# Kernel optimization log

Hardware: AMD Instinct MI355X
Metric: run time of the kernel (lower is better)

Reference implementation:

```python
import jax, jax.numpy as jnp
import numpy as np

LN_EPS = 1e-5


def _ln(x, g, b):
    mu = jnp.mean(x, -1, keepdims=True)
    xc = x - mu
    inv = jax.lax.rsqrt(jnp.mean(xc * xc, -1, keepdims=True) + LN_EPS)
    return xc * inv * g + b


def _subm_conv(x, nbr, W, b):
    # Submanifold 3D conv via rulebook gather-GEMM-accumulate.
    # x: [N, Cin], nbr: [N, K] neighbor row ids (-1 = missing), W: [K, Cin, Cout], b: [Cout]
    N = x.shape[0]
    xp = jnp.concatenate([x, jnp.zeros((1, x.shape[1]), x.dtype)], 0)  # sentinel zero row
    idx = jnp.where(nbr < 0, N, nbr)  # missing neighbors -> zero row
    acc0 = jnp.zeros((N, W.shape[-1]), x.dtype) + b
    def body(acc, xs):
        i, Wk = xs  # i: [N], Wk: [Cin, Cout]
        return acc + xp[i] @ Wk, None
    acc, _ = jax.lax.scan(body, acc0, (idx.T, W))
    return acc


def _blk1(x, W, b, g, be):  # 1x1x1 SubMConv + LN + ReLU
    return jax.nn.relu(_ln(x @ W + b, g, be))


def _blk3(x, nbr, W, b, g, be):  # 3x3x3 SubMConv + LN + ReLU
    return jax.nn.relu(_ln(_subm_conv(x, nbr, W, b), g, be))


def setup_inputs() -> dict:
    rng = np.random.default_rng(0)
    B, D, Npb, K = 2, 160, 131072, 27
    dim, half = 64, 32
    # Build random sparse voxel set and the rulebook (neighbor table) like spconv does.
    lookup = np.full((B, D, D, D), -1, np.int64)
    coords = np.zeros((B * Npb, 3), np.int64)
    for b in range(B):
        lin = np.sort(rng.choice(D * D * D, size=Npb, replace=False))
        z, y, x = np.unravel_index(lin, (D, D, D))
        rows = np.arange(b * Npb, (b + 1) * Npb)
        lookup[b, z, y, x] = rows
        coords[rows] = np.stack([z, y, x], 1)
    bidx = np.repeat(np.arange(B), Npb)
    offs = np.stack(np.meshgrid(np.arange(-1, 2), np.arange(-1, 2), np.arange(-1, 2), indexing="ij"), -1).reshape(K, 3)
    nz = coords[:, None, :] + offs[None]  # [N, K, 3]
    valid = ((nz >= 0) & (nz < D)).all(-1)
    nzc = np.clip(nz, 0, D - 1)
    nbr = lookup[bidx[:, None], nzc[..., 0], nzc[..., 1], nzc[..., 2]]
    nbr = np.where(valid, nbr, -1).astype(np.int32)

    key = jax.random.key(0)
    ks = iter(jax.random.split(key, 16))
    f32 = jnp.float32
    d = {"voxel_features": jax.random.normal(next(ks), (B * Npb, dim), f32),
         "nbr_idx": jnp.asarray(nbr)}
    def lnp(c):
        return jnp.ones((c,), f32), jnp.zeros((c,), f32)
    d["W1"] = 0.05 * jax.random.normal(next(ks), (dim, dim), f32); d["b1"] = jnp.zeros((dim,), f32); d["g1"], d["be1"] = lnp(dim)
    d["W2"] = 0.05 * jax.random.normal(next(ks), (dim, dim), f32); d["b2"] = jnp.zeros((dim,), f32); d["g2"], d["be2"] = lnp(dim)
    d["W3"] = 0.05 * jax.random.normal(next(ks), (K, dim, half), f32); d["b3"] = jnp.zeros((half,), f32); d["g3"], d["be3"] = lnp(half)
    d["W4"] = 0.05 * jax.random.normal(next(ks), (K, half, half), f32); d["b4"] = jnp.zeros((half,), f32); d["g4"], d["be4"] = lnp(half)
    d["W5"] = 0.05 * jax.random.normal(next(ks), (K, half, half), f32); d["b5"] = jnp.zeros((half,), f32); d["g5"], d["be5"] = lnp(half)
    d["W6"] = 0.05 * jax.random.normal(next(ks), (K, half, half), f32); d["b6"] = jnp.zeros((half,), f32); d["g6"], d["be6"] = lnp(half)
    d["W7"] = 0.05 * jax.random.normal(next(ks), (4 * dim, dim), f32); d["b7"] = jnp.zeros((dim,), f32); d["g7"], d["be7"] = lnp(dim)
    return d


def reference(voxel_features, nbr_idx,
              W1, b1, g1, be1, W2, b2, g2, be2,
              W3, b3, g3, be3, W4, b4, g4, be4,
              W5, b5, g5, be5, W6, b6, g6, be6,
              W7, b7, g7, be7):
    x = voxel_features
    f1 = _blk1(x, W1, b1, g1, be1)
    f2 = _blk1(x, W2, b2, g2, be2)
    feats = [f1, f2]
    f2 = _blk3(f2, nbr_idx, W3, b3, g3, be3); feats.append(f2)
    f2 = _blk3(f2, nbr_idx, W4, b4, g4, be4); feats.append(f2)
    f2 = _blk3(f2, nbr_idx, W5, b5, g5, be5); feats.append(f2)
    f2 = _blk3(f2, nbr_idx, W6, b6, g6, be6); feats.append(f2)
    cat = jnp.concatenate(feats, -1)  # [N, 4*dim]
    return _blk1(cat, W7, b7, g7, be7)
```

## Files before the change

### kernel.cpp

```cpp
#include <hip/hip_runtime.h>

typedef __attribute__((ext_vector_type(4))) float  float4_;
typedef __attribute__((ext_vector_type(8))) short  short8;
typedef __attribute__((ext_vector_type(8))) __bf16 bf16x8;
typedef __attribute__((ext_vector_type(4))) unsigned uint4_;

__device__ inline unsigned short f2bf(float f) {
    unsigned u = __builtin_bit_cast(unsigned, f);
    u += 0x7FFFu + ((u >> 16) & 1u);
    return (unsigned short)(u >> 16);
}

__device__ inline float4_ mfma16(bf16x8 a, bf16x8 b, float4_ c) {
    return __builtin_amdgcn_mfma_f32_16x16x32_bf16(a, b, c, 0, 0, 0);
}

__device__ inline void packW_one(const float* __restrict__ src, unsigned short* __restrict__ dst,
                                 int cin, int cout, int e) {
    int f = e >> 9, i = e & 511, lane = i >> 3, t = i & 7;
    int ntn = cout >> 4, ctn = cin >> 5;
    int nt = f % ntn;
    int rest = f / ntn;
    int ct = rest % ctn;
    int k = rest / ctn;
    int c = ct * 32 + (lane >> 4) * 8 + t;
    int j = nt * 16 + (lane & 15);
    dst[e] = f2bf(src[(k * cin + c) * cout + j]);
}

__global__ void pack_all_kernel(
    const float* __restrict__ W1, const float* __restrict__ W2,
    const float* __restrict__ W3, const float* __restrict__ W4,
    const float* __restrict__ W5, const float* __restrict__ W6,
    const float* __restrict__ W7,
    unsigned short* cat, unsigned short* Wp12, unsigned short* Wp3,
    unsigned short* Wp4, unsigned short* Wp5, unsigned short* Wp6,
    unsigned short* Wp7, int N) {
    int e = blockIdx.x * 256 + threadIdx.x;
    if (e < 8192) {
        int f = e >> 9, i = e & 511, lane = i >> 3, t = i & 7;
        int nt = f & 7, ct = f >> 3;
        int c = ct * 32 + (lane >> 4) * 8 + t;
        int j = nt * 16 + (lane & 15);
        float v = (j < 64) ? W1[c * 64 + j] : W2[c * 64 + (j - 64)];
        Wp12[e] = f2bf(v);
        return;
    }
    e -= 8192;
    if (e < 57344) { if (e < 55296) packW_one(W3, Wp3, 64, 32, e); else Wp3[e] = 0; return; }
    e -= 57344;
    if (e < 28672) { if (e < 27648) packW_one(W4, Wp4, 32, 32, e); else Wp4[e] = 0; return; }
    e -= 28672;
    if (e < 28672) { if (e < 27648) packW_one(W5, Wp5, 32, 32, e); else Wp5[e] = 0; return; }
    e -= 28672;
    if (e < 28672) { if (e < 27648) packW_one(W6, Wp6, 32, 32, e); else Wp6[e] = 0; return; }
    e -= 28672;
    if (e < 16384) { packW_one(W7, Wp7, 256, 64, e); return; }
    e -= 16384;
    if (e < 128) ((unsigned*)(cat + (size_t)N * 256))[e] = 0;
}

__global__ __launch_bounds__(256) void plan_kernel(const int* __restrict__ nbr,
                                                   unsigned int* __restrict__ kmask,
                                                   unsigned int* __restrict__ cidx,
                                                   unsigned char* __restrict__ ktab, int N) {
    __shared__ int snb[6912];
    __shared__ unsigned tm[16];
    int tid = threadIdx.x;
    if (tid < 16) tm[tid] = 0u;
    __syncthreads();
    long base = (long)blockIdx.x * 6912;
#pragma unroll
    for (int i = 0; i < 27; i++) {
        int j = i * 256 + tid;
        int v = nbr[base + j];
        snb[j] = v;
        if (v >= 0) {
            unsigned r = (unsigned)j / 27u;
            unsigned k = (unsigned)j - r * 27u;
            atomicOr(&tm[r >> 4], 1u << k);
        }
    }
    __syncthreads();
    int g = tid >> 4, r = tid & 15;
    unsigned m = tm[g];
    int t = blockIdx.x * 16 + g;
    unsigned* cp = cidx + (long)t * 448;
    int j = 0;
#pragma unroll
    for (int k = 0; k < 27; k++) {
        if (m >> k & 1u) {
            int v = snb[(g * 16 + r) * 27 + k];
            cp[j * 16 + r] = (unsigned)(v < 0 ? N : v) * 512u;
            j++;
        }
    }
    for (; j < 28; j++) cp[j * 16 + r] = (unsigned)N * 512u;
    if (r == 0) {
        kmask[t] = m;
        unsigned char* kt = ktab + (long)t * 32;
        int jj = 0;
#pragma unroll
        for (int k = 0; k < 27; k++)
            if (m >> k & 1u) kt[jj++] = (unsigned char)k;
        for (; jj < 32; jj++) kt[jj] = 27;
    }
}

__global__ __launch_bounds__(256) void blk12_kernel(
    const float* __restrict__ x, unsigned short* cat,
    const unsigned short* __restrict__ Wp,
    const float* __restrict__ b1, const float* __restrict__ g1, const float* __restrict__ be1,
    const float* __restrict__ b2, const float* __restrict__ g2, const float* __restrict__ be2) {
    int tid = threadIdx.x, lane = tid & 63, wv = tid >> 6;
    int l15 = lane & 15, q = lane >> 4;
    long base = ((long)blockIdx.x * 4 + wv) * 16;

    float4_ acc[8];
#pragma unroll
    for (int i = 0; i < 8; i++) acc[i] = (float4_){0.f, 0.f, 0.f, 0.f};

#pragma unroll
    for (int kt = 0; kt < 2; kt++) {
        const float* xp = x + (base + l15) * 64 + kt * 32 + q * 8;
        float4_ f0 = *(const float4_*)xp;
        float4_ f1 = *(const float4_*)(xp + 4);
        short8 as;
        as[0] = (short)f2bf(f0[0]); as[1] = (short)f2bf(f0[1]);
        as[2] = (short)f2bf(f0[2]); as[3] = (short)f2bf(f0[3]);
        as[4] = (short)f2bf(f1[0]); as[5] = (short)f2bf(f1[1]);
        as[6] = (short)f2bf(f1[2]); as[7] = (short)f2bf(f1[3]);
        bf16x8 a = __builtin_bit_cast(bf16x8, as);
        const unsigned short* wp = Wp + (size_t)kt * 8 * 512;
#pragma unroll
        for (int nt = 0; nt < 8; nt++) {
            bf16x8 w = *(const bf16x8*)(wp + nt * 512 + lane * 8);
            acc[nt] = mfma16(a, w, acc[nt]);
        }
    }

    float bc[8], gc[8], bec[8];
#pragma unroll
    for (int nt = 0; nt < 8; nt++) {
        int j = nt * 16 + l15;
        if (j < 64) { bc[nt] = b1[j]; gc[nt] = g1[j]; bec[nt] = be1[j]; }
        else        { bc[nt] = b2[j - 64]; gc[nt] = g2[j - 64]; bec[nt] = be2[j - 64]; }
    }

#pragma unroll
    for (int r = 0; r < 4; r++) {
        long row = base + q * 4 + r;
        float v[8], s0 = 0.f, s1 = 0.f, q0 = 0.f, q1 = 0.f;
#pragma unroll
        for (int nt = 0; nt < 4; nt++) { v[nt] = acc[nt][r] + bc[nt]; s0 += v[nt]; q0 += v[nt] * v[nt]; }
#pragma unroll
        for (int nt = 4; nt < 8; nt++) { v[nt] = acc[nt][r] + bc[nt]; s1 += v[nt]; q1 += v[nt] * v[nt]; }
#pragma unroll
        for (int m = 1; m < 16; m <<= 1) {
            s0 += __shfl_xor(s0, m); q0 += __shfl_xor(q0, m);
            s1 += __shfl_xor(s1, m); q1 += __shfl_xor(q1, m);
        }
        float mu0 = s0 * (1.f / 64), var0 = q0 * (1.f / 64) - mu0 * mu0, inv0 = rsqrtf(var0 + 1e-5f);
        float mu1 = s1 * (1.f / 64), var1 = q1 * (1.f / 64) - mu1 * mu1, inv1 = rsqrtf(var1 + 1e-5f);
        unsigned short* cp = cat + row * 256;
#pragma unroll
        for (int nt = 0; nt < 4; nt++) {
            float y = fmaxf((v[nt] - mu0) * inv0 * gc[nt] + bec[nt], 0.f);
            cp[nt * 16 + l15] = f2bf(y);
        }
#pragma unroll
        for (int nt = 4; nt < 8; nt++) {
            float y = fmaxf((v[nt] - mu1) * inv1 * gc[nt] + bec[nt], 0.f);
            cp[nt * 16 + l15] = f2bf(y);
        }
    }
}

template <int CT, int D, int NS>
__device__ __forceinline__ void conv_core(
    float4_ acc[2], const char* catb, const unsigned* cx,
    const unsigned* kt8, const unsigned short* wl) {
    bf16x8 f[D + 1][CT];
    bf16x8 wr[3][CT][2];
    unsigned cv[3];

#define KB(k) ((kt8[(k) >> 2] >> (((k) & 3) * 8)) & 0xFFu)

    unsigned cv0[D + 2];
#pragma unroll
    for (int j = 0; j < D + 2; j++) cv0[j] = cx[j * 16];

#pragma unroll
    for (int kk = 0; kk < 2; kk++) {
        unsigned wo = KB(kk) * (CT * 1024u);
#pragma unroll
        for (int ct = 0; ct < CT; ct++)
#pragma unroll
            for (int nt = 0; nt < 2; nt++)
                wr[kk][ct][nt] = *(const bf16x8*)(wl + wo + (ct * 2 + nt) * 512);
    }

#pragma unroll
    for (int j = 0; j < D; j++) {
#pragma unroll
        for (int ct = 0; ct < CT; ct++)
            f[j][ct] = *(const bf16x8*)(catb + (size_t)cv0[j] + ct * 64);
    }
    cv[D % 3] = cv0[D];
    cv[(D + 1) % 3] = cv0[D + 1];

#pragma unroll
    for (int k = 0; k < NS; k++) {
        if (k + 2 < NS) {
            unsigned wo = KB(k + 2) * (CT * 1024u);
#pragma unroll
            for (int ct = 0; ct < CT; ct++)
#pragma unroll
                for (int nt = 0; nt < 2; nt++)
                    wr[(k + 2) % 3][ct][nt] = *(const bf16x8*)(wl + wo + (ct * 2 + nt) * 512);
        }
        if (k + D < NS) {
            unsigned voff = cv[(k + D) % 3];
#pragma unroll
            for (int ct = 0; ct < CT; ct++)
                f[(k + D) % (D + 1)][ct] = *(const bf16x8*)(catb + (size_t)voff + ct * 64);
        }
        if (k + D + 2 < NS) cv[(k + D + 2) % 3] = cx[(k + D + 2) * 16];
#pragma unroll
        for (int ct = 0; ct < CT; ct++) {
            acc[0] = mfma16(f[k % (D + 1)][ct], wr[k % 3][ct][0], acc[0]);
            acc[1] = mfma16(f[k % (D + 1)][ct], wr[k % 3][ct][1], acc[1]);
        }
    }
#undef KB
}

template <int CT, int D>
__global__ __launch_bounds__(256) void conv_kernel(
    unsigned short* cat, const unsigned int* __restrict__ cidx,
    const unsigned char* __restrict__ ktab,
    const unsigned int* __restrict__ kmask,
    const unsigned short* __restrict__ Wp,
    const float* __restrict__ bb, const float* __restrict__ gg, const float* __restrict__ bee,
    int in_off, int out_off, int N) {
    int tid = threadIdx.x, lane = tid & 63, wv = tid >> 6;
    int l15 = lane & 15, q = lane >> 4;

    int cpx = (int)(gridDim.x >> 3);
    int sb = ((int)blockIdx.x & 7) * cpx + ((int)blockIdx.x >> 3);
    int t = sb * 4 + wv;
    long base = (long)t * 16;

    unsigned m = __builtin_amdgcn_readfirstlane(kmask[t]);
    int trips = (__popc(m) + 3) >> 2;

    const char* catb = (const char*)cat + (size_t)in_off * 2 + q * 16;
    const unsigned* cx = cidx + (long)t * 448 + l15;
    const unsigned short* wl = Wp + lane * 8;

    uint4_ kv0 = *(const uint4_*)(ktab + (long)t * 32);
    uint4_ kv1 = *(const uint4_*)(ktab + (long)t * 32 + 16);
    unsigned kt8[8] = {kv0[0], kv0[1], kv0[2], kv0[3], kv1[0], kv1[1], kv1[2], kv1[3]};

    float4_ acc[2];
    acc[0] = (float4_){0.f, 0.f, 0.f, 0.f};
    acc[1] = (float4_){0.f, 0.f, 0.f, 0.f};

    switch (trips) {
        case 1: conv_core<CT, D, 4>(acc, catb, cx, kt8, wl); break;
        case 2: conv_core<CT, D, 8>(acc, catb, cx, kt8, wl); break;
        case 3: conv_core<CT, D, 12>(acc, catb, cx, kt8, wl); break;
        case 4: conv_core<CT, D, 16>(acc, catb, cx, kt8, wl); break;
        case 5: conv_core<CT, D, 20>(acc, catb, cx, kt8, wl); break;
        case 6: conv_core<CT, D, 24>(acc, catb, cx, kt8, wl); break;
        default: conv_core<CT, D, 28>(acc, catb, cx, kt8, wl); break;
    }

    float b0c = bb[l15], b1c = bb[16 + l15];
    float g0c = gg[l15], g1c = gg[16 + l15];
    float be0c = bee[l15], be1c = bee[16 + l15];

#pragma unroll
    for (int r = 0; r < 4; r++) {
        long row = base + q * 4 + r;
        float v0 = acc[0][r] + b0c;
        float v1 = acc[1][r] + b1c;
        float s = v0 + v1, sq = v0 * v0 + v1 * v1;
#pragma unroll
        for (int mh = 1; mh < 16; mh <<= 1) { s += __shfl_xor(s, mh); sq += __shfl_xor(sq, mh); }
        float mu = s * (1.f / 32), var = sq * (1.f / 32) - mu * mu, inv = rsqrtf(var + 1e-5f);
        float y0 = fmaxf((v0 - mu) * inv * g0c + be0c, 0.f);
        float y1 = fmaxf((v1 - mu) * inv * g1c + be1c, 0.f);
        unsigned short* cp = cat + row * 256 + out_off;
        cp[l15] = f2bf(y0);
        cp[16 + l15] = f2bf(y1);
    }
}

__global__ __launch_bounds__(256) void blk7_kernel(
    const unsigned short* __restrict__ cat, const unsigned short* __restrict__ Wp,
    const float* __restrict__ b, const float* __restrict__ g, const float* __restrict__ be,
    float* __restrict__ out) {
    int tid = threadIdx.x, lane = tid & 63, wv = tid >> 6;
    int l15 = lane & 15, q = lane >> 4;
    long base = ((long)blockIdx.x * 4 + wv) * 16;

    float4_ acc[4];
#pragma unroll
    for (int i = 0; i < 4; i++) acc[i] = (float4_){0.f, 0.f, 0.f, 0.f};

#pragma unroll
    for (int kt = 0; kt < 8; kt++) {
        bf16x8 a = *(const bf16x8*)(cat + (base + l15) * 256 + kt * 32 + q * 8);
        const unsigned short* wp = Wp + (size_t)kt * 4 * 512;
#pragma unroll
        for (int nt = 0; nt < 4; nt++) {
            bf16x8 w = *(const bf16x8*)(wp + nt * 512 + lane * 8);
            acc[nt] = mfma16(a, w, acc[nt]);
        }
    }

    float bc[4], gc[4], bec[4];
#pragma unroll
    for (int nt = 0; nt < 4; nt++) {
        int j = nt * 16 + l15;
        bc[nt] = b[j]; gc[nt] = g[j]; bec[nt] = be[j];
    }

#pragma unroll
    for (int r = 0; r < 4; r++) {
        long row = base + q * 4 + r;
        float v[4], s = 0.f, sq = 0.f;
#pragma unroll
        for (int nt = 0; nt < 4; nt++) { v[nt] = acc[nt][r] + bc[nt]; s += v[nt]; sq += v[nt] * v[nt]; }
#pragma unroll
        for (int m = 1; m < 16; m <<= 1) { s += __shfl_xor(s, m); sq += __shfl_xor(sq, m); }
        float mu = s * (1.f / 64), var = sq * (1.f / 64) - mu * mu, inv = rsqrtf(var + 1e-5f);
#pragma unroll
        for (int nt = 0; nt < 4; nt++) {
            float y = fmaxf((v[nt] - mu) * inv * gc[nt] + bec[nt], 0.f);
            out[row * 64 + nt * 16 + l15] = y;
        }
    }
}

extern "C" void kernel_launch(void* const* d_in, const int* in_sizes, int n_in,
                              void* d_out, int out_size, void* d_ws, size_t ws_size,
                              hipStream_t stream) {
    const int N = in_sizes[0] / 64;

    const float* x   = (const float*)d_in[0];
    const int*   nbr = (const int*)d_in[1];
    const float* W1 = (const float*)d_in[2];
    const float* b1 = (const float*)d_in[3];
    const float* g1 = (const float*)d_in[4];
    const float* be1 = (const float*)d_in[5];
    const float* W2 = (const float*)d_in[6];
    const float* b2 = (const float*)d_in[7];
    const float* g2 = (const float*)d_in[8];
    const float* be2 = (const float*)d_in[9];
    const float* W3 = (const float*)d_in[10];
    const float* b3 = (const float*)d_in[11];
    const float* g3 = (const float*)d_in[12];
    const float* be3 = (const float*)d_in[13];
    const float* W4 = (const float*)d_in[14];
    const float* b4 = (const float*)d_in[15];
    const float* g4 = (const float*)d_in[16];
    const float* be4 = (const float*)d_in[17];
    const float* W5 = (const float*)d_in[18];
    const float* b5 = (const float*)d_in[19];
    const float* g5 = (const float*)d_in[20];
    const float* be5 = (const float*)d_in[21];
    const float* W6 = (const float*)d_in[22];
    const float* b6 = (const float*)d_in[23];
    const float* g6 = (const float*)d_in[24];
    const float* be6 = (const float*)d_in[25];
    const float* W7 = (const float*)d_in[26];
    const float* b7 = (const float*)d_in[27];
    const float* g7 = (const float*)d_in[28];
    const float* be7 = (const float*)d_in[29];

    unsigned short* ws   = (unsigned short*)d_ws;
    unsigned short* cat  = ws;
    unsigned short* Wp12 = cat + (size_t)(N + 1) * 256;
    unsigned short* Wp3  = Wp12 + 8192;
    unsigned short* Wp4  = Wp3 + 57344;
    unsigned short* Wp5  = Wp4 + 28672;
    unsigned short* Wp6  = Wp5 + 28672;
    unsigned short* Wp7  = Wp6 + 28672;
    unsigned int*   kmask = (unsigned int*)(Wp7 + 16384);
    unsigned int*   cidx  = kmask + N / 16;
    unsigned char*  ktab  = (unsigned char*)(cidx + (size_t)(N / 16) * 448);

    pack_all_kernel<<<657, 256, 0, stream>>>(W1, W2, W3, W4, W5, W6, W7,
                                             cat, Wp12, Wp3, Wp4, Wp5, Wp6, Wp7, N);
    plan_kernel<<<N / 256, 256, 0, stream>>>(nbr, kmask, cidx, ktab, N);

    blk12_kernel<<<N / 64, 256, 0, stream>>>(x, cat, Wp12, b1, g1, be1, b2, g2, be2);
    conv_kernel<2, 3><<<N / 64, 256, 0, stream>>>(cat, cidx, ktab, kmask, Wp3, b3, g3, be3, 64, 128, N);
    conv_kernel<1, 4><<<N / 64, 256, 0, stream>>>(cat, cidx, ktab, kmask, Wp4, b4, g4, be4, 128, 160, N);
    conv_kernel<1, 4><<<N / 64, 256, 0, stream>>>(cat, cidx, ktab, kmask, Wp5, b5, g5, be5, 160, 192, N);
    conv_kernel<1, 4><<<N / 64, 256, 0, stream>>>(cat, cidx, ktab, kmask, Wp6, b6, g6, be6, 192, 224, N);
    blk7_kernel<<<N / 64, 256, 0, stream>>>(cat, Wp7, b7, g7, be7, (float*)d_out);
}
```

Before: 434.6 us.

## Preload per-row gather indices as vectors and deepen conv prefetch pipeline

The plan kernel now writes each row's neighbor offsets contiguously, padded to 32 entries. The conv kernel loads all 28 of them up front with seven 16-byte loads instead of issuing a strided scalar load per step. Feature prefetch depth rises from 3/4 to 5/8 stages, and the weight ring gains a buffer for the single-tile case. Together these remove dependent index loads from the inner loop and keep more gathers in flight, at the cost of more VGPRs, possible lower occupancy, and a larger index buffer.

After: 490.6 us. 1.13x slower.

```diff
diff --git a/kernel.cpp b/kernel.cpp
--- a/kernel.cpp
+++ b/kernel.cpp
@@ -85,17 +85,17 @@
     int g = tid >> 4, r = tid & 15;
     unsigned m = tm[g];
     int t = blockIdx.x * 16 + g;
-    unsigned* cp = cidx + (long)t * 448;
+    unsigned* cp = cidx + (size_t)t * 512 + (size_t)r * 32;
     int j = 0;
 #pragma unroll
     for (int k = 0; k < 27; k++) {
         if (m >> k & 1u) {
             int v = snb[(g * 16 + r) * 27 + k];
-            cp[j * 16 + r] = (unsigned)(v < 0 ? N : v) * 512u;
+            cp[j] = (unsigned)(v < 0 ? N : v) * 512u;
             j++;
         }
     }
-    for (; j < 28; j++) cp[j * 16 + r] = (unsigned)N * 512u;
+    for (; j < 28; j++) cp[j] = (unsigned)N * 512u;
     if (r == 0) {
         kmask[t] = m;
         unsigned char* kt = ktab + (long)t * 32;
@@ -178,20 +178,18 @@
 
 template <int CT, int D, int NS>
 __device__ __forceinline__ void conv_core(
-    float4_ acc[2], const char* catb, const unsigned* cx,
+    float4_ acc[2], const char* catb, const uint4_* iv,
     const unsigned* kt8, const unsigned short* wl) {
     bf16x8 f[D + 1][CT];
-    bf16x8 wr[3][CT][2];
-    unsigned cv[3];
+    constexpr int WR = (CT == 1) ? 4 : 3;
+    constexpr int WL = WR - 1;
+    bf16x8 wr[WR][CT][2];
 
 #define KB(k) ((kt8[(k) >> 2] >> (((k) & 3) * 8)) & 0xFFu)
-
-    unsigned cv0[D + 2];
-#pragma unroll
-    for (int j = 0; j < D + 2; j++) cv0[j] = cx[j * 16];
-
-#pragma unroll
-    for (int kk = 0; kk < 2; kk++) {
+#define IDX(j) (iv[(j) >> 2][(j) & 3])
+
+#pragma unroll
+    for (int kk = 0; kk < WL; kk++) {
         unsigned wo = KB(kk) * (CT * 1024u);
 #pragma unroll
         for (int ct = 0; ct < CT; ct++)
@@ -199,39 +197,36 @@
             for (int nt = 0; nt < 2; nt++)
                 wr[kk][ct][nt] = *(const bf16x8*)(wl + wo + (ct * 2 + nt) * 512);
     }
-
 #pragma unroll
     for (int j = 0; j < D; j++) {
 #pragma unroll
         for (int ct = 0; ct < CT; ct++)
-            f[j][ct] = *(const bf16x8*)(catb + (size_t)cv0[j] + ct * 64);
-    }
-    cv[D % 3] = cv0[D];
-    cv[(D + 1) % 3] = cv0[D + 1];
+            f[j][ct] = *(const bf16x8*)(catb + (size_t)IDX(j) + ct * 64);
+    }
 
 #pragma unroll
     for (int k = 0; k < NS; k++) {
-        if (k + 2 < NS) {
-            unsigned wo = KB(k + 2) * (CT * 1024u);
+        if (k + WL < NS) {
+            unsigned wo = KB(k + WL) * (CT * 1024u);
 #pragma unroll
             for (int ct = 0; ct < CT; ct++)
 #pragma unroll
                 for (int nt = 0; nt < 2; nt++)
-                    wr[(k + 2) % 3][ct][nt] = *(const bf16x8*)(wl + wo + (ct * 2 + nt) * 512);
+                    wr[(k + WL) % WR][ct][nt] = *(const bf16x8*)(wl + wo + (ct * 2 + nt) * 512);
         }
         if (k + D < NS) {
-            unsigned voff = cv[(k + D) % 3];
+            unsigned voff = IDX(k + D);
 #pragma unroll
             for (int ct = 0; ct < CT; ct++)
                 f[(k + D) % (D + 1)][ct] = *(const bf16x8*)(catb + (size_t)voff + ct * 64);
         }
-        if (k + D + 2 < NS) cv[(k + D + 2) % 3] = cx[(k + D + 2) * 16];
 #pragma unroll
         for (int ct = 0; ct < CT; ct++) {
-            acc[0] = mfma16(f[k % (D + 1)][ct], wr[k % 3][ct][0], acc[0]);
-            acc[1] = mfma16(f[k % (D + 1)][ct], wr[k % 3][ct][1], acc[1]);
-        }
-    }
+            acc[0] = mfma16(f[k % (D + 1)][ct], wr[k % WR][ct][0], acc[0]);
+            acc[1] = mfma16(f[k % (D + 1)][ct], wr[k % WR][ct][1], acc[1]);
+        }
+    }
+#undef IDX
 #undef KB
 }
 
@@ -255,8 +250,12 @@
     int trips = (__popc(m) + 3) >> 2;
 
     const char* catb = (const char*)cat + (size_t)in_off * 2 + q * 16;
-    const unsigned* cx = cidx + (long)t * 448 + l15;
     const unsigned short* wl = Wp + lane * 8;
+
+    const unsigned* cxr = cidx + (size_t)t * 512 + (size_t)l15 * 32;
+    uint4_ iv[7];
+#pragma unroll
+    for (int i = 0; i < 7; i++) iv[i] = *(const uint4_*)(cxr + i * 4);
 
     uint4_ kv0 = *(const uint4_*)(ktab + (long)t * 32);
     uint4_ kv1 = *(const uint4_*)(ktab + (long)t * 32 + 16);
@@ -267,13 +266,13 @@
     acc[1] = (float4_){0.f, 0.f, 0.f, 0.f};
 
     switch (trips) {
-        case 1: conv_core<CT, D, 4>(acc, catb, cx, kt8, wl); break;
-        case 2: conv_core<CT, D, 8>(acc, catb, cx, kt8, wl); break;
-        case 3: conv_core<CT, D, 12>(acc, catb, cx, kt8, wl); break;
-        case 4: conv_core<CT, D, 16>(acc, catb, cx, kt8, wl); break;
-        case 5: conv_core<CT, D, 20>(acc, catb, cx, kt8, wl); break;
-        case 6: conv_core<CT, D, 24>(acc, catb, cx, kt8, wl); break;
-        default: conv_core<CT, D, 28>(acc, catb, cx, kt8, wl); break;
+        case 1: conv_core<CT, D, 4>(acc, catb, iv, kt8, wl); break;
+        case 2: conv_core<CT, D, 8>(acc, catb, iv, kt8, wl); break;
+        case 3: conv_core<CT, D, 12>(acc, catb, iv, kt8, wl); break;
+        case 4: conv_core<CT, D, 16>(acc, catb, iv, kt8, wl); break;
+        case 5: conv_core<CT, D, 20>(acc, catb, iv, kt8, wl); break;
+        case 6: conv_core<CT, D, 24>(acc, catb, iv, kt8, wl); break;
+        default: conv_core<CT, D, 28>(acc, catb, iv, kt8, wl); break;
     }
 
     float b0c = bb[l15], b1c = bb[16 + l15];
@@ -390,16 +389,16 @@
     unsigned short* Wp7  = Wp6 + 28672;
     unsigned int*   kmask = (unsigned int*)(Wp7 + 16384);
     unsigned int*   cidx  = kmask + N / 16;
-    unsigned char*  ktab  = (unsigned char*)(cidx + (size_t)(N / 16) * 448);
+    unsigned char*  ktab  = (unsigned char*)(cidx + (size_t)(N / 16) * 512);
 
     pack_all_kernel<<<657, 256, 0, stream>>>(W1, W2, W3, W4, W5, W6, W7,
                                              cat, Wp12, Wp3, Wp4, Wp5, Wp6, Wp7, N);
     plan_kernel<<<N / 256, 256, 0, stream>>>(nbr, kmask, cidx, ktab, N);
 
     blk12_kernel<<<N / 64, 256, 0, stream>>>(x, cat, Wp12, b1, g1, be1, b2, g2, be2);
-    conv_kernel<2, 3><<<N / 64, 256, 0, stream>>>(cat, cidx, ktab, kmask, Wp3, b3, g3, be3, 64, 128, N);
-    conv_kernel<1, 4><<<N / 64, 256, 0, stream>>>(cat, cidx, ktab, kmask, Wp4, b4, g4, be4, 128, 160, N);
-    conv_kernel<1, 4><<<N / 64, 256, 0, stream>>>(cat, cidx, ktab, kmask, Wp5, b5, g5, be5, 160, 192, N);
-    conv_kernel<1, 4><<<N / 64, 256, 0, stream>>>(cat, cidx, ktab, kmask, Wp6, b6, g6, be6, 192, 224, N);
+    conv_kernel<2, 5><<<N / 64, 256, 0, stream>>>(cat, cidx, ktab, kmask, Wp3, b3, g3, be3, 64, 128, N);
+    conv_kernel<1, 8><<<N / 64, 256, 0, stream>>>(cat, cidx, ktab, kmask, Wp4, b4, g4, be4, 128, 160, N);
+    conv_kernel<1, 8><<<N / 64, 256, 0, stream>>>(cat, cidx, ktab, kmask, Wp5, b5, g5, be5, 160, 192, N);
+    conv_kernel<1, 8><<<N / 64, 256, 0, stream>>>(cat, cidx, ktab, kmask, Wp6, b6, g6, be6, 192, 224, N);
     blk7_kernel<<<N / 64, 256, 0, stream>>>(cat, Wp7, b7, g7, be7, (float*)d_out);
 }
```
